# Kernel tuning notes

Measured on AMD Instinct MI355X. Metric: run time of the kernel, lower is better.

## Reference

```python
import jax, jax.numpy as jnp
import numpy as np

N = 50000      # nodes
E = 800000     # edges (avg degree 16)
IN = 128
H = 128
OUT = 1000
K = 10
EPS = 1e-5


def setup_inputs() -> dict:
    key = jax.random.key(0)
    ks = jax.random.split(key, 12)
    s = 0.05  # small init scale for weights
    return {
        "x": jax.random.normal(ks[0], (N, IN), jnp.float32),
        "edge_index": jax.random.randint(ks[1], (2, E), 0, N, dtype=jnp.int32),
        "W1": jax.random.normal(ks[2], (IN, H), jnp.float32) * s,
        "b1": jnp.zeros((H,), jnp.float32),
        "g1": jnp.ones((H,), jnp.float32),
        "be1": jnp.zeros((H,), jnp.float32),
        "W2": jax.random.normal(ks[3], (H, H), jnp.float32) * s,
        "b2": jnp.zeros((H,), jnp.float32),
        "g2": jnp.ones((H,), jnp.float32),
        "be2": jnp.zeros((H,), jnp.float32),
        "att": jax.random.uniform(ks[4], (K + 1,), jnp.float32),  # uniform_(0,1) init
        "W3": jax.random.normal(ks[5], (H, H // 2), jnp.float32) * s,
        "b3": jnp.zeros((H // 2,), jnp.float32),
        "g3": jnp.ones((H // 2,), jnp.float32),
        "be3": jnp.zeros((H // 2,), jnp.float32),
        "Wout": jax.random.normal(ks[6], (H // 2, OUT), jnp.float32) * s,
        "bout": jnp.zeros((OUT,), jnp.float32),
    }


def _bn(x, g, b):
    # training-mode BatchNorm1d: biased batch stats over the node dim
    m = jnp.mean(x, axis=0)
    v = jnp.var(x, axis=0)
    return g * (x - m) * jax.lax.rsqrt(v + EPS) + b


def reference(x, edge_index, W1, b1, g1, be1, W2, b2, g2, be2, att,
              W3, b3, g3, be3, Wout, bout):
    # input MLP with residual
    h = jax.nn.relu(_bn(x @ W1 + b1, g1, be1))
    identity = h
    h = jax.nn.relu(_bn(h @ W2 + b2, g2, be2)) + identity

    # DAGNN: K unnormalized scatter-add hops (APPNP.propagate with edge_weight=1),
    # then softmax(att)-weighted sum over hop representations. Accumulate the
    # weighted sum on the fly instead of materializing the [N, H, K+1] stack.
    src, dst = edge_index[0], edge_index[1]  # message flows src -> dst
    w = jax.nn.softmax(att)
    out = w[0] * h
    cur = h
    for i in range(K):
        cur = jax.ops.segment_sum(cur[src], dst, num_segments=N)
        out = out + w[i + 1] * cur

    # output MLP
    h3 = jax.nn.relu(_bn(out @ W3 + b3, g3, be3))
    return h3 @ Wout + bout
```

## Files before the change

### kernel.cpp

```cpp
#include <hip/hip_runtime.h>
#include <cstdint>
#include <cstddef>

#define N_NODES 50000
#define N_EDGES 800000
#define DIM_H   128
#define DIM_P   64
#define DIM_OUT 1000
#define OUT_PAD 1024
#define KHOPS   10
#define BN_EPS  1e-5f

static inline int ceil_div(int a, int b) { return (a + b - 1) / b; }

typedef short  bf16x8  __attribute__((ext_vector_type(8)));
typedef float  floatx4 __attribute__((ext_vector_type(4)));

__device__ __forceinline__ unsigned short f2bf_rne(float v) {
    unsigned int u = __float_as_uint(v);
    return (unsigned short)((u + 0x7fffu + ((u >> 16) & 1u)) >> 16);
}

__global__ void softmax11(const float* __restrict__ att, float* __restrict__ w) {
    if (threadIdx.x == 0) {
        float mx = att[0];
        for (int i = 1; i < KHOPS + 1; ++i) mx = fmaxf(mx, att[i]);
        float e[KHOPS + 1];
        float s = 0.f;
        for (int i = 0; i < KHOPS + 1; ++i) { e[i] = expf(att[i] - mx); s += e[i]; }
        for (int i = 0; i < KHOPS + 1; ++i) w[i] = e[i] / s;
    }
}

__global__ void count_deg(const int* __restrict__ dst, int* __restrict__ deg, int ne) {
    int i = blockIdx.x * blockDim.x + threadIdx.x;
    if (i < ne) atomicAdd(&deg[dst[i]], 1);
}

__global__ __launch_bounds__(1024) void scan_local(const int* __restrict__ deg,
                                                   int* __restrict__ row_ptr,
                                                   int* __restrict__ bsums, int n) {
    __shared__ int wsum[16];
    const int i = blockIdx.x * 1024 + threadIdx.x;
    const int lane = threadIdx.x & 63, w = threadIdx.x >> 6;
    int v = (i < n) ? deg[i] : 0;
    int s = v;
#pragma unroll
    for (int d = 1; d < 64; d <<= 1) {
        int t = __shfl_up(s, d, 64);
        if (lane >= d) s += t;
    }
    if (lane == 63) wsum[w] = s;
    __syncthreads();
    if (w == 0) {
        int x = (lane < 16) ? wsum[lane] : 0;
#pragma unroll
        for (int d = 1; d < 16; d <<= 1) {
            int t = __shfl_up(x, d, 64);
            if (lane >= d) x += t;
        }
        if (lane < 16) wsum[lane] = x;
    }
    __syncthreads();
    int incl = s + ((w > 0) ? wsum[w - 1] : 0);
    if (i < n) row_ptr[i + 1] = incl;
    if (threadIdx.x == 1023) bsums[blockIdx.x] = incl;
}

__global__ void scan_bsums(int* __restrict__ bsums, int nb) {
    int lane = threadIdx.x;
    int v = (lane < nb) ? bsums[lane] : 0;
    int s = v;
#pragma unroll
    for (int d = 1; d < 64; d <<= 1) {
        int t = __shfl_up(s, d, 64);
        if (lane >= d) s += t;
    }
    if (lane < nb) bsums[lane] = s - v;
}

__global__ void scan_finish(int* __restrict__ row_ptr, int* __restrict__ deg,
                            const int* __restrict__ bsums, int n) {
    int i = blockIdx.x * blockDim.x + threadIdx.x;
    if (i < n) {
        int incl = row_ptr[i + 1] + bsums[i >> 10];
        row_ptr[i + 1] = incl;
        deg[i] = incl - deg[i];
    }
    if (i == 0) row_ptr[0] = 0;
}

__global__ void fill_csr(const int* __restrict__ src, const int* __restrict__ dst,
                         int* __restrict__ cursor, int* __restrict__ col, int ne) {
    int i = blockIdx.x * blockDim.x + threadIdx.x;
    if (i < ne) {
        int d = dst[i];
        int pos = atomicAdd(&cursor[d], 1);
        col[pos] = src[i];
    }
}

template<int KD, int CPB>
__global__ __launch_bounds__(256) void gemm_fused(
    const float* __restrict__ A,  const float* __restrict__ scA,
    const float* __restrict__ A2, const float* __restrict__ scA2,
    const float* __restrict__ W,  const float* __restrict__ bias,
    float* __restrict__ C, float* __restrict__ C2, const float* __restrict__ w0p,
    int n, int M) {
    constexpr int CG  = CPB / 4;
    constexpr int RG  = 256 / CG;
    constexpr int RPT = 64 / RG;
    __shared__ float As[64][KD + 4];

    const int tid  = threadIdx.x;
    const int cg   = tid % CG;
    const int rg   = tid / CG;
    const int row0 = blockIdx.x * 64;
    const int col0 = blockIdx.y * CPB + cg * 4;

    constexpr int VECS = 64 * KD / 4;
    for (int i = tid; i < VECS; i += 256) {
        int r  = i / (KD / 4);
        int k4 = (i % (KD / 4)) * 4;
        float4 v = make_float4(0.f, 0.f, 0.f, 0.f);
        int row = row0 + r;
        if (row < n) {
            v = *reinterpret_cast<const float4*>(A + (size_t)row * KD + k4);
            if (scA) {
                float4 sc = *reinterpret_cast<const float4*>(scA + k4);
                float4 sh = *reinterpret_cast<const float4*>(scA + KD + k4);
                v.x = fmaxf(v.x * sc.x + sh.x, 0.f);
                v.y = fmaxf(v.y * sc.y + sh.y, 0.f);
                v.z = fmaxf(v.z * sc.z + sh.z, 0.f);
                v.w = fmaxf(v.w * sc.w + sh.w, 0.f);
            }
            if (A2) {
                float4 u  = *reinterpret_cast<const float4*>(A2 + (size_t)row * KD + k4);
                float4 sc = *reinterpret_cast<const float4*>(scA2 + k4);
                float4 sh = *reinterpret_cast<const float4*>(scA2 + KD + k4);
                v.x += fmaxf(u.x * sc.x + sh.x, 0.f);
                v.y += fmaxf(u.y * sc.y + sh.y, 0.f);
                v.z += fmaxf(u.z * sc.z + sh.z, 0.f);
                v.w += fmaxf(u.w * sc.w + sh.w, 0.f);
            }
        }
        *reinterpret_cast<float4*>(&As[r][k4]) = v;
    }
    __syncthreads();

    if (col0 >= M) return;

    float acc[RPT][4];
#pragma unroll
    for (int r = 0; r < RPT; ++r)
#pragma unroll
        for (int c = 0; c < 4; ++c) acc[r][c] = 0.f;

    for (int k4 = 0; k4 < KD; k4 += 4) {
        float4 w0 = *reinterpret_cast<const float4*>(W + (size_t)(k4 + 0) * M + col0);
        float4 w1 = *reinterpret_cast<const float4*>(W + (size_t)(k4 + 1) * M + col0);
        float4 w2 = *reinterpret_cast<const float4*>(W + (size_t)(k4 + 2) * M + col0);
        float4 w3 = *reinterpret_cast<const float4*>(W + (size_t)(k4 + 3) * M + col0);
#pragma unroll
        for (int r = 0; r < RPT; ++r) {
            float4 a = *reinterpret_cast<const float4*>(&As[rg * RPT + r][k4]);
            acc[r][0] += a.x * w0.x + a.y * w1.x + a.z * w2.x + a.w * w3.x;
            acc[r][1] += a.x * w0.y + a.y * w1.y + a.z * w2.y + a.w * w3.y;
            acc[r][2] += a.x * w0.z + a.y * w1.z + a.z * w2.z + a.w * w3.z;
            acc[r][3] += a.x * w0.w + a.y * w1.w + a.z * w2.w + a.w * w3.w;
        }
    }

    float4 b = make_float4(0.f, 0.f, 0.f, 0.f);
    if (bias) b = *reinterpret_cast<const float4*>(bias + col0);
    const float w0s = C2 ? w0p[0] : 0.f;
#pragma unroll
    for (int r = 0; r < RPT; ++r) {
        int row = row0 + rg * RPT + r;
        if (row < n) {
            float4 o = make_float4(acc[r][0] + b.x, acc[r][1] + b.y,
                                   acc[r][2] + b.z, acc[r][3] + b.w);
            *reinterpret_cast<float4*>(C + (size_t)row * M + col0) = o;
            if (C2) {
                float4 q = make_float4(w0s * o.x, w0s * o.y, w0s * o.z, w0s * o.w);
                *reinterpret_cast<float4*>(C2 + (size_t)row * M + col0) = q;
            }
        }
    }
}

template<int M>
__global__ __launch_bounds__(256) void colstats(const float* __restrict__ Z,
                                                double* __restrict__ st, int n) {
    constexpr int RG = 256 / M;
    const int tid = threadIdx.x;
    const int c = tid % M, rg = tid / M;
    double s = 0.0, ss = 0.0;
    for (int row = blockIdx.x * RG + rg; row < n; row += gridDim.x * RG) {
        float v = Z[(size_t)row * M + c];
        s += v;
        ss += (double)v * (double)v;
    }
    __shared__ double sh[2][256];
    sh[0][tid] = s;
    sh[1][tid] = ss;
    __syncthreads();
    if (rg == 0) {
#pragma unroll
        for (int g = 1; g < RG; ++g) { s += sh[0][c + g * M]; ss += sh[1][c + g * M]; }
        atomicAdd(&st[c], s);
        atomicAdd(&st[M + c], ss);
    }
}

__global__ void bn_finalize(const double* __restrict__ st, const float* __restrict__ g,
                            const float* __restrict__ be, float* __restrict__ scsh,
                            int M, int n) {
    int c = threadIdx.x + blockIdx.x * blockDim.x;
    if (c < M) {
        double m = st[c] / n;
        double v = st[M + c] / n - m * m;
        float scale = g[c] * rsqrtf((float)v + BN_EPS);
        scsh[c]     = scale;
        scsh[M + c] = be[c] - (float)m * scale;
    }
}

__global__ __launch_bounds__(256) void propagate(
    const float* __restrict__ cur, float* __restrict__ nxt, float* __restrict__ oacc,
    const int* __restrict__ row_ptr, const int* __restrict__ col,
    const float* __restrict__ wts, int hop, int n) {
    const int node = blockIdx.x * 4 + (threadIdx.x >> 6);
    const int lane = threadIdx.x & 63;
    const int g = lane >> 4;
    const int l = lane & 15;
    if (node >= n) return;
    const int beg = row_ptr[node], end = row_ptr[node + 1];
    float4 acc = make_float4(0.f, 0.f, 0.f, 0.f);
    int e = beg;
    for (; e + 8 <= end; e += 8) {
        int s0 = col[e + g];
        int s1 = col[e + g + 4];
        float4 v0 = *reinterpret_cast<const float4*>(cur + (size_t)s0 * DIM_P + l * 4);
        float4 v1 = *reinterpret_cast<const float4*>(cur + (size_t)s1 * DIM_P + l * 4);
        acc.x += v0.x + v1.x; acc.y += v0.y + v1.y;
        acc.z += v0.z + v1.z; acc.w += v0.w + v1.w;
    }
    if (e + 4 <= end) {
        int s = col[e + g];
        float4 v = *reinterpret_cast<const float4*>(cur + (size_t)s * DIM_P + l * 4);
        acc.x += v.x; acc.y += v.y; acc.z += v.z; acc.w += v.w;
        e += 4;
    }
    if (e + g < end) {
        int s = col[e + g];
        float4 v = *reinterpret_cast<const float4*>(cur + (size_t)s * DIM_P + l * 4);
        acc.x += v.x; acc.y += v.y; acc.z += v.z; acc.w += v.w;
    }
#pragma unroll
    for (int off = 16; off < 64; off <<= 1) {
        acc.x += __shfl_xor(acc.x, off, 64);
        acc.y += __shfl_xor(acc.y, off, 64);
        acc.z += __shfl_xor(acc.z, off, 64);
        acc.w += __shfl_xor(acc.w, off, 64);
    }
    if (g == 0) {
        size_t o = (size_t)node * DIM_P + l * 4;
        if (nxt) *reinterpret_cast<float4*>(nxt + o) = acc;
        const float w = wts[hop];
        float4 t = *reinterpret_cast<const float4*>(oacc + o);
        t.x = fmaf(w, acc.x, t.x); t.y = fmaf(w, acc.y, t.y);
        t.z = fmaf(w, acc.z, t.z); t.w = fmaf(w, acc.w, t.w);
        *reinterpret_cast<float4*>(oacc + o) = t;
    }
}

__global__ void prep_wout(const float* __restrict__ W, unsigned short* __restrict__ WT) {
    int idx = blockIdx.x * blockDim.x + threadIdx.x;
    if (idx < OUT_PAD * DIM_P) {
        int c = idx >> 6, k = idx & 63;
        WT[idx] = (c < DIM_OUT) ? f2bf_rne(W[(size_t)k * DIM_OUT + c]) : (unsigned short)0;
    }
}

__global__ void bn3_relu_bf16(const float* __restrict__ Z, const float* __restrict__ scsh,
                              unsigned short* __restrict__ O) {
    const int total8 = N_NODES * DIM_P / 8;
    int i = blockIdx.x * blockDim.x + threadIdx.x;
    if (i >= total8) return;
    int base = i * 8;
    int c = base & (DIM_P - 1);
    float4 z0 = *reinterpret_cast<const float4*>(Z + base);
    float4 z1 = *reinterpret_cast<const float4*>(Z + base + 4);
    float4 s0 = *reinterpret_cast<const float4*>(scsh + c);
    float4 s1 = *reinterpret_cast<const float4*>(scsh + c + 4);
    float4 h0 = *reinterpret_cast<const float4*>(scsh + DIM_P + c);
    float4 h1 = *reinterpret_cast<const float4*>(scsh + DIM_P + c + 4);
    bf16x8 o;
    o[0] = (short)f2bf_rne(fmaxf(z0.x * s0.x + h0.x, 0.f));
    o[1] = (short)f2bf_rne(fmaxf(z0.y * s0.y + h0.y, 0.f));
    o[2] = (short)f2bf_rne(fmaxf(z0.z * s0.z + h0.z, 0.f));
    o[3] = (short)f2bf_rne(fmaxf(z0.w * s0.w + h0.w, 0.f));
    o[4] = (short)f2bf_rne(fmaxf(z1.x * s1.x + h1.x, 0.f));
    o[5] = (short)f2bf_rne(fmaxf(z1.y * s1.y + h1.y, 0.f));
    o[6] = (short)f2bf_rne(fmaxf(z1.z * s1.z + h1.z, 0.f));
    o[7] = (short)f2bf_rne(fmaxf(z1.w * s1.w + h1.w, 0.f));
    *reinterpret_cast<bf16x8*>(O + base) = o;
}

__global__ __launch_bounds__(256, 4) void out_gemm_mfma(
    const unsigned short* __restrict__ ABF, const unsigned short* __restrict__ WT,
    const float* __restrict__ bout, float* __restrict__ out) {
    const int wave = threadIdx.x >> 6;
    const int lane = threadIdx.x & 63;
    const int m    = lane & 15;
    const int quad = lane >> 4;
    const int kb   = quad * 8;
    const int c0   = blockIdx.y * 256 + wave * 64;

    bf16x8 afrag[4][2];
    float4 bias[4];
#pragma unroll
    for (int t = 0; t < 4; ++t) {
        const unsigned short* wrow = WT + (size_t)(c0 + t * 16 + m) * DIM_P;
        afrag[t][0] = *reinterpret_cast<const bf16x8*>(wrow + kb);
        afrag[t][1] = *reinterpret_cast<const bf16x8*>(wrow + 32 + kb);
        int cc = c0 + t * 16 + quad * 4;
        bias[t] = (cc < DIM_OUT) ? *reinterpret_cast<const float4*>(bout + cc)
                                 : make_float4(0.f, 0.f, 0.f, 0.f);
    }

    const int NT = N_NODES / 16;
    for (int rt = blockIdx.x; rt < NT; rt += gridDim.x) {
        const int row = rt * 16 + m;
        const unsigned short* arow = ABF + (size_t)row * DIM_P;
        bf16x8 bfrag0 = *reinterpret_cast<const bf16x8*>(arow + kb);
        bf16x8 bfrag1 = *reinterpret_cast<const bf16x8*>(arow + 32 + kb);
        float* orow = out + (size_t)row * DIM_OUT;
#pragma unroll
        for (int t = 0; t < 4; ++t) {
            floatx4 acc = {0.f, 0.f, 0.f, 0.f};
            acc = __builtin_amdgcn_mfma_f32_16x16x32_bf16(afrag[t][0], bfrag0, acc, 0, 0, 0);
            acc = __builtin_amdgcn_mfma_f32_16x16x32_bf16(afrag[t][1], bfrag1, acc, 0, 0, 0);
            int cc = c0 + t * 16 + quad * 4;
            if (cc < DIM_OUT) {
                float4 o = make_float4(acc[0] + bias[t].x, acc[1] + bias[t].y,
                                       acc[2] + bias[t].z, acc[3] + bias[t].w);
                *reinterpret_cast<float4*>(orow + cc) = o;
            }
        }
    }
}

extern "C" void kernel_launch(void* const* d_in, const int* in_sizes, int n_in,
                              void* d_out, int out_size, void* d_ws, size_t ws_size,
                              hipStream_t stream) {
    const float* x    = (const float*)d_in[0];
    const int*   ei   = (const int*)  d_in[1];
    const float* W1   = (const float*)d_in[2];
    const float* g1   = (const float*)d_in[4];
    const float* be1  = (const float*)d_in[5];
    const float* W2   = (const float*)d_in[6];
    const float* g2   = (const float*)d_in[8];
    const float* be2  = (const float*)d_in[9];
    const float* att  = (const float*)d_in[10];
    const float* W3   = (const float*)d_in[11];
    const float* g3   = (const float*)d_in[13];
    const float* be3  = (const float*)d_in[14];
    const float* Wout = (const float*)d_in[15];
    const float* bout = (const float*)d_in[16];
    float* out = (float*)d_out;

    char* base = (char*)d_ws;
    size_t off = 0;
    auto alloc = [&](size_t bytes) -> void* {
        void* r = base + off;
        off += (bytes + 255) & ~(size_t)255;
        return r;
    };
    float*  f0      = (float*) alloc((size_t)N_NODES * DIM_H * 4);
    float*  f1      = (float*) alloc((size_t)N_NODES * DIM_H * 4);
    float*  yb      = (float*) alloc((size_t)N_NODES * DIM_P * 4);
    float*  tb      = (float*) alloc((size_t)N_NODES * DIM_P * 4);
    float*  oa      = (float*) alloc((size_t)N_NODES * DIM_P * 4);
    double* st      = (double*)alloc(640 * 8);
    float*  scsh    = (float*) alloc(768 * 4);
    float*  wts     = (float*) alloc(16 * 4);
    int*    row_ptr = (int*)   alloc((size_t)(N_NODES + 1) * 4);
    int*    deg     = (int*)   alloc((size_t)N_NODES * 4);
    int*    col     = (int*)   alloc((size_t)N_EDGES * 4);
    int*    bsums   = (int*)   alloc(64 * 4);
    unsigned short* WT  = (unsigned short*)alloc((size_t)OUT_PAD * DIM_P * 2);
    unsigned short* ABF = (unsigned short*)alloc((size_t)N_NODES * DIM_P * 2);

    const int* src = ei;
    const int* dst = ei + N_EDGES;
    double* st1 = st;   double* st2 = st + 256; double* st3 = st + 512;
    float*  sc1 = scsh; float*  sc2 = scsh + 256; float* sc3 = scsh + 512;

    hipMemsetAsync(st, 0, 640 * 8, stream);
    hipMemsetAsync(deg, 0, (size_t)N_NODES * 4, stream);

    softmax11<<<1, 64, 0, stream>>>(att, wts);
    prep_wout<<<ceil_div(OUT_PAD * DIM_P, 256), 256, 0, stream>>>(Wout, WT);

    count_deg<<<ceil_div(N_EDGES, 256), 256, 0, stream>>>(dst, deg, N_EDGES);
    const int NB = ceil_div(N_NODES, 1024);
    scan_local<<<NB, 1024, 0, stream>>>(deg, row_ptr, bsums, N_NODES);
    scan_bsums<<<1, 64, 0, stream>>>(bsums, NB);
    scan_finish<<<ceil_div(N_NODES, 256), 256, 0, stream>>>(row_ptr, deg, bsums, N_NODES);
    fill_csr<<<ceil_div(N_EDGES, 256), 256, 0, stream>>>(src, dst, deg, col, N_EDGES);

    const int RB = ceil_div(N_NODES, 64);

    gemm_fused<128, 128><<<dim3(RB, 1), 256, 0, stream>>>(
        x, nullptr, nullptr, nullptr, W1, nullptr, f0, nullptr, nullptr, N_NODES, DIM_H);
    colstats<128><<<256, 256, 0, stream>>>(f0, st1, N_NODES);
    bn_finalize<<<1, 128, 0, stream>>>(st1, g1, be1, sc1, 128, N_NODES);

    gemm_fused<128, 128><<<dim3(RB, 1), 256, 0, stream>>>(
        f0, sc1, nullptr, nullptr, W2, nullptr, f1, nullptr, nullptr, N_NODES, DIM_H);
    colstats<128><<<256, 256, 0, stream>>>(f1, st2, N_NODES);
    bn_finalize<<<1, 128, 0, stream>>>(st2, g2, be2, sc2, 128, N_NODES);

    gemm_fused<128, 64><<<dim3(RB, 1), 256, 0, stream>>>(
        f1, sc2, f0, sc1, W3, nullptr, yb, oa, wts, N_NODES, DIM_P);

    float* cur = yb;
    float* nxt = tb;
    for (int hop = 1; hop <= KHOPS; ++hop) {
        propagate<<<ceil_div(N_NODES, 4), 256, 0, stream>>>(
            cur, (hop == KHOPS) ? nullptr : nxt, oa, row_ptr, col, wts, hop, N_NODES);
        float* t = cur; cur = nxt; nxt = t;
    }

    colstats<64><<<256, 256, 0, stream>>>(oa, st3, N_NODES);
    bn_finalize<<<1, 64, 0, stream>>>(st3, g3, be3, sc3, 64, N_NODES);
    bn3_relu_bf16<<<ceil_div(N_NODES * DIM_P / 8, 256), 256, 0, stream>>>(oa, sc3, ABF);

    out_gemm_mfma<<<dim3(512, 4), 256, 0, stream>>>(ABF, WT, bout, out);
}
```

Measured before the change: 874.6 us.

## Fuse BN column stats into GEMM epilogue and batch neighbor index loads

Adds a STATS template flag so the first two GEMMs reduce per-column sums and sums of squares in shared memory and atomically add them in double. This removes the two separate colstats passes that re-read the full activation matrices. Separately, the propagate kernel now loads up to 64 neighbor indices per wave in one coalesced read, broadcasts them with shuffles, and issues four gathers per iteration with masking, aiming for more memory-level parallelism. The stats are now accumulated in float per block before the double atomics, which slightly changes numerical precision, and the masked gather loop adds some wasted loads on low-degree nodes.

```diff
diff --git a/kernel.cpp b/kernel.cpp
--- a/kernel.cpp
+++ b/kernel.cpp
@@ -100,13 +100,13 @@
     }
 }
 
-template<int KD, int CPB>
+template<int KD, int CPB, bool STATS>
 __global__ __launch_bounds__(256) void gemm_fused(
     const float* __restrict__ A,  const float* __restrict__ scA,
     const float* __restrict__ A2, const float* __restrict__ scA2,
     const float* __restrict__ W,  const float* __restrict__ bias,
     float* __restrict__ C, float* __restrict__ C2, const float* __restrict__ w0p,
-    int n, int M) {
+    double* __restrict__ st, int n, int M) {
     constexpr int CG  = CPB / 4;
     constexpr int RG  = 256 / CG;
     constexpr int RPT = 64 / RG;
@@ -148,42 +148,80 @@
     }
     __syncthreads();
 
-    if (col0 >= M) return;
-
     float acc[RPT][4];
 #pragma unroll
     for (int r = 0; r < RPT; ++r)
 #pragma unroll
         for (int c = 0; c < 4; ++c) acc[r][c] = 0.f;
 
-    for (int k4 = 0; k4 < KD; k4 += 4) {
-        float4 w0 = *reinterpret_cast<const float4*>(W + (size_t)(k4 + 0) * M + col0);
-        float4 w1 = *reinterpret_cast<const float4*>(W + (size_t)(k4 + 1) * M + col0);
-        float4 w2 = *reinterpret_cast<const float4*>(W + (size_t)(k4 + 2) * M + col0);
-        float4 w3 = *reinterpret_cast<const float4*>(W + (size_t)(k4 + 3) * M + col0);
+    if (col0 < M) {
+        for (int k4 = 0; k4 < KD; k4 += 4) {
+            float4 w0 = *reinterpret_cast<const float4*>(W + (size_t)(k4 + 0) * M + col0);
+            float4 w1 = *reinterpret_cast<const float4*>(W + (size_t)(k4 + 1) * M + col0);
+            float4 w2 = *reinterpret_cast<const float4*>(W + (size_t)(k4 + 2) * M + col0);
+            float4 w3 = *reinterpret_cast<const float4*>(W + (size_t)(k4 + 3) * M + col0);
+#pragma unroll
+            for (int r = 0; r < RPT; ++r) {
+                float4 a = *reinterpret_cast<const float4*>(&As[rg * RPT + r][k4]);
+                acc[r][0] += a.x * w0.x + a.y * w1.x + a.z * w2.x + a.w * w3.x;
+                acc[r][1] += a.x * w0.y + a.y * w1.y + a.z * w2.y + a.w * w3.y;
+                acc[r][2] += a.x * w0.z + a.y * w1.z + a.z * w2.z + a.w * w3.z;
+                acc[r][3] += a.x * w0.w + a.y * w1.w + a.z * w2.w + a.w * w3.w;
+            }
+        }
+
+        float4 b = make_float4(0.f, 0.f, 0.f, 0.f);
+        if (bias) b = *reinterpret_cast<const float4*>(bias + col0);
+        const float w0s = C2 ? w0p[0] : 0.f;
 #pragma unroll
         for (int r = 0; r < RPT; ++r) {
-            float4 a = *reinterpret_cast<const float4*>(&As[rg * RPT + r][k4]);
-            acc[r][0] += a.x * w0.x + a.y * w1.x + a.z * w2.x + a.w * w3.x;
-            acc[r][1] += a.x * w0.y + a.y * w1.y + a.z * w2.y + a.w * w3.y;
-            acc[r][2] += a.x * w0.z + a.y * w1.z + a.z * w2.z + a.w * w3.z;
-            acc[r][3] += a.x * w0.w + a.y * w1.w + a.z * w2.w + a.w * w3.w;
-        }
-    }
-
-    float4 b = make_float4(0.f, 0.f, 0.f, 0.f);
-    if (bias) b = *reinterpret_cast<const float4*>(bias + col0);
-    const float w0s = C2 ? w0p[0] : 0.f;
-#pragma unroll
-    for (int r = 0; r < RPT; ++r) {
-        int row = row0 + rg * RPT + r;
-        if (row < n) {
-            float4 o = make_float4(acc[r][0] + b.x, acc[r][1] + b.y,
-                                   acc[r][2] + b.z, acc[r][3] + b.w);
-            *reinterpret_cast<float4*>(C + (size_t)row * M + col0) = o;
-            if (C2) {
-                float4 q = make_float4(w0s * o.x, w0s * o.y, w0s * o.z, w0s * o.w);
-                *reinterpret_cast<float4*>(C2 + (size_t)row * M + col0) = q;
+            int row = row0 + rg * RPT + r;
+            if (row < n) {
+                float4 o = make_float4(acc[r][0] + b.x, acc[r][1] + b.y,
+                                       acc[r][2] + b.z, acc[r][3] + b.w);
+                *reinterpret_cast<float4*>(C + (size_t)row * M + col0) = o;
+                if (C2) {
+                    float4 q = make_float4(w0s * o.x, w0s * o.y, w0s * o.z, w0s * o.w);
+                    *reinterpret_cast<float4*>(C2 + (size_t)row * M + col0) = q;
+                }
+            }
+        }
+    }
+
+    if (STATS) {
+        float s[4] = {0.f, 0.f, 0.f, 0.f}, q[4] = {0.f, 0.f, 0.f, 0.f};
+#pragma unroll
+        for (int r = 0; r < RPT; ++r) {
+            int row = row0 + rg * RPT + r;
+            if (row < n) {
+#pragma unroll
+                for (int c = 0; c < 4; ++c) {
+                    float v = acc[r][c];
+                    s[c] += v;
+                    q[c] += v * v;
+                }
+            }
+        }
+        __syncthreads();
+        float* sb = &As[0][0];
+        float* qb = sb + RG * CPB;
+#pragma unroll
+        for (int c = 0; c < 4; ++c) {
+            sb[rg * CPB + cg * 4 + c] = s[c];
+            qb[rg * CPB + cg * 4 + c] = q[c];
+        }
+        __syncthreads();
+        if (rg == 0 && col0 < M) {
+#pragma unroll
+            for (int c = 0; c < 4; ++c) {
+                float ts = 0.f, tq = 0.f;
+#pragma unroll
+                for (int g2 = 0; g2 < RG; ++g2) {
+                    ts += sb[g2 * CPB + cg * 4 + c];
+                    tq += qb[g2 * CPB + cg * 4 + c];
+                }
+                atomicAdd(&st[col0 + c], (double)ts);
+                atomicAdd(&st[M + col0 + c], (double)tq);
             }
         }
     }
@@ -237,25 +275,29 @@
     if (node >= n) return;
     const int beg = row_ptr[node], end = row_ptr[node + 1];
     float4 acc = make_float4(0.f, 0.f, 0.f, 0.f);
-    int e = beg;
-    for (; e + 8 <= end; e += 8) {
-        int s0 = col[e + g];
-        int s1 = col[e + g + 4];
-        float4 v0 = *reinterpret_cast<const float4*>(cur + (size_t)s0 * DIM_P + l * 4);
-        float4 v1 = *reinterpret_cast<const float4*>(cur + (size_t)s1 * DIM_P + l * 4);
-        acc.x += v0.x + v1.x; acc.y += v0.y + v1.y;
-        acc.z += v0.z + v1.z; acc.w += v0.w + v1.w;
-    }
-    if (e + 4 <= end) {
-        int s = col[e + g];
-        float4 v = *reinterpret_cast<const float4*>(cur + (size_t)s * DIM_P + l * 4);
-        acc.x += v.x; acc.y += v.y; acc.z += v.z; acc.w += v.w;
-        e += 4;
-    }
-    if (e + g < end) {
-        int s = col[e + g];
-        float4 v = *reinterpret_cast<const float4*>(cur + (size_t)s * DIM_P + l * 4);
-        acc.x += v.x; acc.y += v.y; acc.z += v.z; acc.w += v.w;
+    for (int base = beg; base < end; base += 64) {
+        const int rem = end - base;
+        int idx = (lane < rem) ? col[base + lane] : 0;
+#pragma unroll 1
+        for (int p = 0; p < 16 && p * 4 < rem; p += 4) {
+            const int e0 = p * 4 + g, e1 = e0 + 4, e2 = e0 + 8, e3 = e0 + 12;
+            const int i0 = __shfl(idx, e0, 64);
+            const int i1 = __shfl(idx, e1, 64);
+            const int i2 = __shfl(idx, e2, 64);
+            const int i3 = __shfl(idx, e3, 64);
+            float4 v0 = *reinterpret_cast<const float4*>(cur + (size_t)i0 * DIM_P + l * 4);
+            float4 v1 = *reinterpret_cast<const float4*>(cur + (size_t)i1 * DIM_P + l * 4);
+            float4 v2 = *reinterpret_cast<const float4*>(cur + (size_t)i2 * DIM_P + l * 4);
+            float4 v3 = *reinterpret_cast<const float4*>(cur + (size_t)i3 * DIM_P + l * 4);
+            const float m0 = (e0 < rem) ? 1.f : 0.f;
+            const float m1 = (e1 < rem) ? 1.f : 0.f;
+            const float m2 = (e2 < rem) ? 1.f : 0.f;
+            const float m3 = (e3 < rem) ? 1.f : 0.f;
+            acc.x += v0.x * m0 + v1.x * m1 + v2.x * m2 + v3.x * m3;
+            acc.y += v0.y * m0 + v1.y * m1 + v2.y * m2 + v3.y * m3;
+            acc.z += v0.z * m0 + v1.z * m1 + v2.z * m2 + v3.z * m3;
+            acc.w += v0.w * m0 + v1.w * m1 + v2.w * m2 + v3.w * m3;
+        }
     }
 #pragma unroll
     for (int off = 16; off < 64; off <<= 1) {
@@ -413,18 +455,18 @@
 
     const int RB = ceil_div(N_NODES, 64);
 
-    gemm_fused<128, 128><<<dim3(RB, 1), 256, 0, stream>>>(
-        x, nullptr, nullptr, nullptr, W1, nullptr, f0, nullptr, nullptr, N_NODES, DIM_H);
-    colstats<128><<<256, 256, 0, stream>>>(f0, st1, N_NODES);
+    gemm_fused<128, 128, true><<<dim3(RB, 1), 256, 0, stream>>>(
+        x, nullptr, nullptr, nullptr, W1, nullptr, f0, nullptr, nullptr, st1,
+        N_NODES, DIM_H);
     bn_finalize<<<1, 128, 0, stream>>>(st1, g1, be1, sc1, 128, N_NODES);
 
-    gemm_fused<128, 128><<<dim3(RB, 1), 256, 0, stream>>>(
-        f0, sc1, nullptr, nullptr, W2, nullptr, f1, nullptr, nullptr, N_NODES, DIM_H);
-    colstats<128><<<256, 256, 0, stream>>>(f1, st2, N_NODES);
+    gemm_fused<128, 128, true><<<dim3(RB, 1), 256, 0, stream>>>(
+        f0, sc1, nullptr, nullptr, W2, nullptr, f1, nullptr, nullptr, st2,
+        N_NODES, DIM_H);
     bn_finalize<<<1, 128, 0, stream>>>(st2, g2, be2, sc2, 128, N_NODES);
 
-    gemm_fused<128, 64><<<dim3(RB, 1), 256, 0, stream>>>(
-        f1, sc2, f0, sc1, W3, nullptr, yb, oa, wts, N_NODES, DIM_P);
+    gemm_fused<128, 64, false><<<dim3(RB, 1), 256, 0, stream>>>(
+        f1, sc2, f0, sc1, W3, nullptr, yb, oa, wts, nullptr, N_NODES, DIM_P);
 
     float* cur = yb;
     float* nxt = tb;
```

Result: slower. 937.8 us (+7.2%).

## Partition propagated features into 8-column slices for cache-resident gathers

Applied to the files above, without the earlier changes.

Stores the 64-wide propagated features as eight column-blocked slices of 8 floats per node, each slice contiguous over all nodes. The propagate kernel now handles one slice per block group and uses one wave per node, with 32 edges gathered in parallel as 32-byte reads, so each slice's working set (about 1.6 MB) can stay in cache. The stats and BN/bf16 conversion kernels are adapted to the blocked layout. The trade-off is that CSR indices are reread eight times per hop, and each gather is only 32 bytes, which lowers the bytes moved per memory request.

```diff
diff --git a/kernel.cpp b/kernel.cpp
--- a/kernel.cpp
+++ b/kernel.cpp
@@ -100,7 +100,7 @@
     }
 }
 
-template<int KD, int CPB>
+template<int KD, int CPB, bool BLK>
 __global__ __launch_bounds__(256) void gemm_fused(
     const float* __restrict__ A,  const float* __restrict__ scA,
     const float* __restrict__ A2, const float* __restrict__ scA2,
@@ -180,10 +180,16 @@
         if (row < n) {
             float4 o = make_float4(acc[r][0] + b.x, acc[r][1] + b.y,
                                    acc[r][2] + b.z, acc[r][3] + b.w);
-            *reinterpret_cast<float4*>(C + (size_t)row * M + col0) = o;
+            size_t oaddr;
+            if (BLK) {
+                oaddr = (size_t)(col0 >> 3) * ((size_t)n * 8) + (size_t)row * 8 + (col0 & 7);
+            } else {
+                oaddr = (size_t)row * M + col0;
+            }
+            *reinterpret_cast<float4*>(C + oaddr) = o;
             if (C2) {
                 float4 q = make_float4(w0s * o.x, w0s * o.y, w0s * o.z, w0s * o.w);
-                *reinterpret_cast<float4*>(C2 + (size_t)row * M + col0) = q;
+                *reinterpret_cast<float4*>(C2 + oaddr) = q;
             }
         }
     }
@@ -213,6 +219,30 @@
     }
 }
 
+__global__ __launch_bounds__(256) void colstats64_blk(const float* __restrict__ Z,
+                                                      double* __restrict__ st, int n) {
+    const int tid = threadIdx.x;
+    const int c = tid & 63, rg = tid >> 6;
+    const int blk = c >> 3, j = c & 7;
+    const float* base = Z + (size_t)blk * (size_t)n * 8 + j;
+    double s = 0.0, ss = 0.0;
+    for (int row = blockIdx.x * 4 + rg; row < n; row += gridDim.x * 4) {
+        float v = base[(size_t)row * 8];
+        s += v;
+        ss += (double)v * (double)v;
+    }
+    __shared__ double sh[2][256];
+    sh[0][tid] = s;
+    sh[1][tid] = ss;
+    __syncthreads();
+    if (rg == 0) {
+#pragma unroll
+        for (int g2 = 1; g2 < 4; ++g2) { s += sh[0][c + g2 * 64]; ss += sh[1][c + g2 * 64]; }
+        atomicAdd(&st[c], s);
+        atomicAdd(&st[64 + c], ss);
+    }
+}
+
 __global__ void bn_finalize(const double* __restrict__ st, const float* __restrict__ g,
                             const float* __restrict__ be, float* __restrict__ scsh,
                             int M, int n) {
@@ -226,52 +256,46 @@
     }
 }
 
-__global__ __launch_bounds__(256) void propagate(
+__global__ __launch_bounds__(256) void propagate_blk(
     const float* __restrict__ cur, float* __restrict__ nxt, float* __restrict__ oacc,
     const int* __restrict__ row_ptr, const int* __restrict__ col,
     const float* __restrict__ wts, int hop, int n) {
-    const int node = blockIdx.x * 4 + (threadIdx.x >> 6);
+    const int slice   = blockIdx.x & 7;
+    const int chunk   = blockIdx.x >> 3;
+    const int nchunks = gridDim.x >> 3;
+    const int wv   = threadIdx.x >> 6;
     const int lane = threadIdx.x & 63;
-    const int g = lane >> 4;
-    const int l = lane & 15;
-    if (node >= n) return;
-    const int beg = row_ptr[node], end = row_ptr[node + 1];
-    float4 acc = make_float4(0.f, 0.f, 0.f, 0.f);
-    int e = beg;
-    for (; e + 8 <= end; e += 8) {
-        int s0 = col[e + g];
-        int s1 = col[e + g + 4];
-        float4 v0 = *reinterpret_cast<const float4*>(cur + (size_t)s0 * DIM_P + l * 4);
-        float4 v1 = *reinterpret_cast<const float4*>(cur + (size_t)s1 * DIM_P + l * 4);
-        acc.x += v0.x + v1.x; acc.y += v0.y + v1.y;
-        acc.z += v0.z + v1.z; acc.w += v0.w + v1.w;
-    }
-    if (e + 4 <= end) {
-        int s = col[e + g];
-        float4 v = *reinterpret_cast<const float4*>(cur + (size_t)s * DIM_P + l * 4);
-        acc.x += v.x; acc.y += v.y; acc.z += v.z; acc.w += v.w;
-        e += 4;
-    }
-    if (e + g < end) {
-        int s = col[e + g];
-        float4 v = *reinterpret_cast<const float4*>(cur + (size_t)s * DIM_P + l * 4);
-        acc.x += v.x; acc.y += v.y; acc.z += v.z; acc.w += v.w;
-    }
-#pragma unroll
-    for (int off = 16; off < 64; off <<= 1) {
-        acc.x += __shfl_xor(acc.x, off, 64);
-        acc.y += __shfl_xor(acc.y, off, 64);
-        acc.z += __shfl_xor(acc.z, off, 64);
-        acc.w += __shfl_xor(acc.w, off, 64);
-    }
-    if (g == 0) {
-        size_t o = (size_t)node * DIM_P + l * 4;
-        if (nxt) *reinterpret_cast<float4*>(nxt + o) = acc;
-        const float w = wts[hop];
-        float4 t = *reinterpret_cast<const float4*>(oacc + o);
-        t.x = fmaf(w, acc.x, t.x); t.y = fmaf(w, acc.y, t.y);
-        t.z = fmaf(w, acc.z, t.z); t.w = fmaf(w, acc.w, t.w);
-        *reinterpret_cast<float4*>(oacc + o) = t;
+    const int g = lane >> 1;
+    const int l = lane & 1;
+    const float w = wts[hop];
+    const size_t sbase = (size_t)slice * (size_t)n * 8;
+
+    for (int node = chunk * 4 + wv; node < n; node += nchunks * 4) {
+        const int beg = row_ptr[node], end = row_ptr[node + 1];
+        float ax = 0.f, ay = 0.f, az = 0.f, aw = 0.f;
+        for (int e = beg; e + g < end; e += 32) {
+            int s = col[e + g];
+            float4 v = *reinterpret_cast<const float4*>(cur + sbase + (size_t)s * 8 + l * 4);
+            ax += v.x; ay += v.y; az += v.z; aw += v.w;
+        }
+#pragma unroll
+        for (int off = 2; off < 64; off <<= 1) {
+            ax += __shfl_xor(ax, off, 64);
+            ay += __shfl_xor(ay, off, 64);
+            az += __shfl_xor(az, off, 64);
+            aw += __shfl_xor(aw, off, 64);
+        }
+        if (g == 0) {
+            size_t o = sbase + (size_t)node * 8 + l * 4;
+            if (nxt) {
+                float4 s4 = make_float4(ax, ay, az, aw);
+                *reinterpret_cast<float4*>(nxt + o) = s4;
+            }
+            float4 t = *reinterpret_cast<const float4*>(oacc + o);
+            t.x = fmaf(w, ax, t.x); t.y = fmaf(w, ay, t.y);
+            t.z = fmaf(w, az, t.z); t.w = fmaf(w, aw, t.w);
+            *reinterpret_cast<float4*>(oacc + o) = t;
+        }
     }
 }
 
@@ -283,15 +307,15 @@
     }
 }
 
-__global__ void bn3_relu_bf16(const float* __restrict__ Z, const float* __restrict__ scsh,
-                              unsigned short* __restrict__ O) {
-    const int total8 = N_NODES * DIM_P / 8;
+__global__ void bn3_relu_bf16_blk(const float* __restrict__ Z, const float* __restrict__ scsh,
+                                  unsigned short* __restrict__ O, int n) {
     int i = blockIdx.x * blockDim.x + threadIdx.x;
-    if (i >= total8) return;
-    int base = i * 8;
-    int c = base & (DIM_P - 1);
-    float4 z0 = *reinterpret_cast<const float4*>(Z + base);
-    float4 z1 = *reinterpret_cast<const float4*>(Z + base + 4);
+    if (i >= n * 8) return;
+    int row = i >> 3, blk = i & 7;
+    const float* zp = Z + (size_t)blk * (size_t)n * 8 + (size_t)row * 8;
+    float4 z0 = *reinterpret_cast<const float4*>(zp);
+    float4 z1 = *reinterpret_cast<const float4*>(zp + 4);
+    int c = blk * 8;
     float4 s0 = *reinterpret_cast<const float4*>(scsh + c);
     float4 s1 = *reinterpret_cast<const float4*>(scsh + c + 4);
     float4 h0 = *reinterpret_cast<const float4*>(scsh + DIM_P + c);
@@ -305,7 +329,7 @@
     o[5] = (short)f2bf_rne(fmaxf(z1.y * s1.y + h1.y, 0.f));
     o[6] = (short)f2bf_rne(fmaxf(z1.z * s1.z + h1.z, 0.f));
     o[7] = (short)f2bf_rne(fmaxf(z1.w * s1.w + h1.w, 0.f));
-    *reinterpret_cast<bf16x8*>(O + base) = o;
+    *reinterpret_cast<bf16x8*>(O + (size_t)row * 64 + blk * 8) = o;
 }
 
 __global__ __launch_bounds__(256, 4) void out_gemm_mfma(
@@ -413,30 +437,33 @@
 
     const int RB = ceil_div(N_NODES, 64);
 
-    gemm_fused<128, 128><<<dim3(RB, 1), 256, 0, stream>>>(
+    gemm_fused<128, 128, false><<<dim3(RB, 1), 256, 0, stream>>>(
         x, nullptr, nullptr, nullptr, W1, nullptr, f0, nullptr, nullptr, N_NODES, DIM_H);
     colstats<128><<<256, 256, 0, stream>>>(f0, st1, N_NODES);
     bn_finalize<<<1, 128, 0, stream>>>(st1, g1, be1, sc1, 128, N_NODES);
 
-    gemm_fused<128, 128><<<dim3(RB, 1), 256, 0, stream>>>(
+    gemm_fused<128, 128, false><<<dim3(RB, 1), 256, 0, stream>>>(
         f0, sc1, nullptr, nullptr, W2, nullptr, f1, nullptr, nullptr, N_NODES, DIM_H);
     colstats<128><<<256, 256, 0, stream>>>(f1, st2, N_NODES);
     bn_finalize<<<1, 128, 0, stream>>>(st2, g2, be2, sc2, 128, N_NODES);
 
-    gemm_fused<128, 64><<<dim3(RB, 1), 256, 0, stream>>>(
+    gemm_fused<128, 64, true><<<dim3(RB, 1), 256, 0, stream>>>(
         f1, sc2, f0, sc1, W3, nullptr, yb, oa, wts, N_NODES, DIM_P);
 
-    float* cur = yb;
-    float* nxt = tb;
-    for (int hop = 1; hop <= KHOPS; ++hop) {
-        propagate<<<ceil_div(N_NODES, 4), 256, 0, stream>>>(
-            cur, (hop == KHOPS) ? nullptr : nxt, oa, row_ptr, col, wts, hop, N_NODES);
-        float* t = cur; cur = nxt; nxt = t;
-    }
-
-    colstats<64><<<256, 256, 0, stream>>>(oa, st3, N_NODES);
+    {
+        const int PBLK = 4096;
+        float* cur = yb;
+        float* nxt = tb;
+        for (int hop = 1; hop <= KHOPS; ++hop) {
+            propagate_blk<<<dim3(8 * PBLK), 256, 0, stream>>>(
+                cur, (hop == KHOPS) ? nullptr : nxt, oa, row_ptr, col, wts, hop, N_NODES);
+            float* t = cur; cur = nxt; nxt = t;
+        }
+    }
+
+    colstats64_blk<<<256, 256, 0, stream>>>(oa, st3, N_NODES);
     bn_finalize<<<1, 64, 0, stream>>>(st3, g3, be3, sc3, 64, N_NODES);
-    bn3_relu_bf16<<<ceil_div(N_NODES * DIM_P / 8, 256), 256, 0, stream>>>(oa, sc3, ABF);
+    bn3_relu_bf16_blk<<<ceil_div(N_NODES * 8, 256), 256, 0, stream>>>(oa, sc3, ABF, N_NODES);
 
     out_gemm_mfma<<<dim3(512, 4), 256, 0, stream>>>(ABF, WT, bout, out);
 }
```

Measured after the change: 1.506 ms. 72.2% more time.
